# Kernel tuning notes

Measured on AMD Instinct MI355X. Metric: run time of the kernel, lower is better.

The kernel has to match this reference:

```python
import jax, jax.numpy as jnp
import numpy as np

OBJECTNESS_LIMIT = 0.7
NUM_ANCHORS = 9
DN = ('NHWC', 'HWIO', 'NHWC')


def _conv(x, w, b):
    return jax.lax.conv_general_dilated(x, w, (1, 1), 'SAME', dimension_numbers=DN) + b


def setup_inputs() -> dict:
    key = jax.random.key(0)
    ks = jax.random.split(key, 4)
    B, H, W, Cin = 4, 256, 256, 64
    x = jax.random.normal(ks[0], (B, H, W, Cin), dtype=jnp.float32)
    # base: Conv2D(512, 3x3, relu, kernel_initializer='normal')
    w_base = jax.random.normal(ks[1], (3, 3, Cin, 512), dtype=jnp.float32) * 0.02
    b_base = jnp.zeros((512,), dtype=jnp.float32)
    # classifier: Conv2D(9, 1x1, sigmoid, kernel_initializer='uniform')
    w_cls = jax.random.uniform(ks[2], (1, 1, 512, NUM_ANCHORS), dtype=jnp.float32, minval=-0.05, maxval=0.05)
    b_cls = jnp.zeros((NUM_ANCHORS,), dtype=jnp.float32)
    w_reg = jax.random.normal(ks[3], (1, 1, 512, 4 * NUM_ANCHORS), dtype=jnp.float32) * 0.02
    b_reg = jnp.zeros((4 * NUM_ANCHORS,), dtype=jnp.float32)
    return {"x": x, "w_base": w_base, "b_base": b_base,
            "w_cls": w_cls, "b_cls": b_cls, "w_reg": w_reg, "b_reg": b_reg}


def reference(x, w_base, b_base, w_cls, b_cls, w_reg, b_reg):
    # shared 3x3 conv trunk
    feat = jax.nn.relu(_conv(x, w_base, b_base))                 # [B,H,W,512]
    # per-anchor objectness
    scores = jax.nn.sigmoid(_conv(feat, w_cls, b_cls))           # [B,H,W,A]
    deltas = _conv(feat, w_reg, b_reg)                           # [B,H,W,4A]
    B, H, W, A = scores.shape
    # vectorized form of the per-anchor threshold loop: keep deltas only
    # where objectness > limit (gather/filter expressed as a mask)
    mask = (scores > OBJECTNESS_LIMIT).astype(deltas.dtype)      # [B,H,W,A]
    masked = (deltas.reshape(B, H, W, A, 4) * mask[..., None]).reshape(B, H, W, 4 * A)
    return jnp.concatenate([scores, masked], axis=-1)            # [B,H,W,5A]
```

## Files before the change

kernel.cpp:

```cpp
#include <hip/hip_runtime.h>
#include <hip/hip_bf16.h>
#include <math.h>


typedef _Float16 fp16x8 __attribute__((ext_vector_type(8)));
typedef _Float16 fp16x4 __attribute__((ext_vector_type(4)));
typedef float    f32x4  __attribute__((ext_vector_type(4)));

#define BT_ELEMS  (18 * 32 * 64 * 8)
#define BT2_ELEMS (48 * 512)
#define BS_BYTES  32768

__global__ __launch_bounds__(256) void rpn_prep(
    const float* __restrict__ wb,
    const float* __restrict__ wc,
    const float* __restrict__ wr,
    _Float16* __restrict__ btI,
    _Float16* __restrict__ bt2_hi, _Float16* __restrict__ bt2_lo)
{
    int t = blockIdx.x * 256 + threadIdx.x;
    if (t < BT_ELEMS) {
        int e    = t & 7;
        int lane = (t >> 3) & 63;
        int j    = (t >> 9) & 31;
        int s    = t >> 14;
        int wv   = j >> 3, l = j & 7;
        int lr   = lane & 15, q = lane >> 4;
        int n    = wv * 128 + l * 16 + lr;
        int k    = s * 32 + q * 8 + e;
        int tap  = k >> 6, c = k & 63;
        btI[t] = (_Float16)wb[(tap * 64 + c) * 512 + n];
    } else if (t < BT_ELEMS + BT2_ELEMS) {
        int jj = t - BT_ELEMS;
        int k = jj & 511;
        int o = jj >> 9;
        float v = 0.f;
        if (o < 9)       v = wc[k * 9 + o];
        else if (o < 45) v = wr[k * 36 + (o - 9)];
        _Float16 h = (_Float16)v;
        bt2_hi[jj] = h;
        bt2_lo[jj] = (_Float16)(v - (float)h);
    }
}

#define FB_OFF      6144
#define FB_PER_WAVE 4608
#define ARENA_BYTES 24576

#define TRUNK_STEP(S, BREG)                                                   \
    {                                                                         \
        const int tap_ = (S) >> 1;                                            \
        const int ky_  = tap_ / 3;                                            \
        const int kx_  = tap_ - ky_ * 3;                                      \
        const int c0_  = ((S) & 1) * 32 + q * 8;                              \
        fp16x8 ah[2];                                                         \
        _Pragma("unroll")                                                     \
        for (int km = 0; km < 2; ++km) {                                      \
            int rowp = km + ky_;                                              \
            int pos  = lr + kx_;                                              \
            ah[km] = *(const fp16x8*)&xs_hi[(rowp * 18 + pos) * 72 + c0_];    \
        }                                                                     \
        _Pragma("unroll")                                                     \
        for (int l = 0; l < 8; ++l) {                                         \
            acc[0][l] = __builtin_amdgcn_mfma_f32_16x16x32_f16(ah[0], BREG[l], acc[0][l], 0, 0, 0); \
            acc[1][l] = __builtin_amdgcn_mfma_f32_16x16x32_f16(ah[1], BREG[l], acc[1][l], 0, 0, 0); \
        }                                                                     \
    }

__global__ __launch_bounds__(256, 3) void rpn_main(
    const float* __restrict__ x,
    const float* __restrict__ b_base,
    const float* __restrict__ b_cls,
    const float* __restrict__ b_reg,
    const _Float16* __restrict__ btI,
    const _Float16* __restrict__ bt2_hi, const _Float16* __restrict__ bt2_lo,
    float* __restrict__ out)
{
    __shared__ char smem[ARENA_BYTES];
    _Float16* xs_hi = (_Float16*)smem;
    float*    zbuf  = (float*)smem;

    const int tid  = threadIdx.x;
    const int wave = tid >> 6;
    const int lane = tid & 63;
    const int q    = lane >> 4;
    const int lr   = lane & 15;
    const int n0   = wave * 128;

    const int wg  = blockIdx.x;
    const int b   = wg >> 11;
    const int rem = wg & 2047;
    const int h0  = (rem >> 4) * 2;
    const int w0  = (rem & 15) * 16;

    const char* gW = (const char*)btI + wave * 8192 + lane * 16;

    fp16x8 bA[8], bB[8];
    #pragma unroll
    for (int l = 0; l < 8; ++l)
        bA[l] = *(const fp16x8*)(gW + (size_t)l * 1024);

    for (int i = 0; i < 5; ++i) {
        int flat = tid + i * 256;
        if (flat < 4 * 18 * 16) {
            int cq  = flat & 15;
            int rp  = flat >> 4;
            int row = rp / 18;
            int pos = rp - row * 18;
            int hh  = h0 - 1 + row;
            int ww  = w0 - 1 + pos;
            fp16x4 h4;
            if (hh >= 0 && hh < 256 && ww >= 0 && ww < 256) {
                const float4 v = *(const float4*)&x[(((b * 256 + hh) * 256 + ww) * 64 + cq * 4)];
                h4[0] = (_Float16)v.x; h4[1] = (_Float16)v.y;
                h4[2] = (_Float16)v.z; h4[3] = (_Float16)v.w;
            } else {
                #pragma unroll
                for (int j = 0; j < 4; ++j) h4[j] = (_Float16)0.f;
            }
            *(fp16x4*)&xs_hi[(row * 18 + pos) * 72 + cq * 4] = h4;
        }
    }
    __syncthreads();

    f32x4 acc[2][8];
    #pragma unroll
    for (int km = 0; km < 2; ++km)
        #pragma unroll
        for (int l = 0; l < 8; ++l)
            acc[km][l] = (f32x4){0.f, 0.f, 0.f, 0.f};

    for (int s = 0; s < 18; s += 2) {
        {
            const char* g1 = gW + (size_t)(s + 1) * BS_BYTES;
            #pragma unroll
            for (int l = 0; l < 8; ++l)
                bB[l] = *(const fp16x8*)(g1 + (size_t)l * 1024);
        }
        TRUNK_STEP(s, bA);
        if (s + 2 < 18) {
            const char* g2 = gW + (size_t)(s + 2) * BS_BYTES;
            #pragma unroll
            for (int l = 0; l < 8; ++l)
                bA[l] = *(const fp16x8*)(g2 + (size_t)l * 1024);
        }
        TRUNK_STEP(s + 1, bB);
    }

    __syncthreads();

    _Float16* fh = (_Float16*)(smem + FB_OFF + wave * FB_PER_WAVE);
    _Float16* fl = fh + 32 * 36;

    f32x4 acc2[2][3];
    #pragma unroll
    for (int km = 0; km < 2; ++km)
        #pragma unroll
        for (int ns = 0; ns < 3; ++ns)
            acc2[km][ns] = (f32x4){0.f, 0.f, 0.f, 0.f};

    for (int sub = 0; sub < 4; ++sub) {
        #pragma unroll
        for (int lh = 0; lh < 2; ++lh) {
            int l = sub * 2 + lh;
            float bias = b_base[n0 + l * 16 + lr];
            #pragma unroll
            for (int km = 0; km < 2; ++km) {
                #pragma unroll
                for (int r = 0; r < 4; ++r) {
                    float v = acc[km][l][r] + bias;
                    v = v > 0.f ? v : 0.f;
                    _Float16 h = (_Float16)v;
                    int row = km * 16 + q * 4 + r;
                    int col = lh * 16 + lr;
                    fh[row * 36 + col] = h;
                    fl[row * 36 + col] = (_Float16)(v - (float)h);
                }
            }
        }
        asm volatile("s_waitcnt lgkmcnt(0)" ::: "memory");

        fp16x8 fah[2], fal[2];
        #pragma unroll
        for (int km = 0; km < 2; ++km) {
            int off = (km * 16 + lr) * 36 + q * 8;
            union { fp16x8 v8; fp16x4 v4[2]; } uh, ul;
            uh.v4[0] = *(const fp16x4*)&fh[off];
            uh.v4[1] = *(const fp16x4*)&fh[off + 4];
            ul.v4[0] = *(const fp16x4*)&fl[off];
            ul.v4[1] = *(const fp16x4*)&fl[off + 4];
            fah[km] = uh.v8;
            fal[km] = ul.v8;
        }

        const int kg = n0 + sub * 32 + q * 8;
        {
            int eo = (0 * 16 + lr) * 512 + kg;
            fp16x8 wh = *(const fp16x8*)&bt2_hi[eo];
            fp16x8 wl = *(const fp16x8*)&bt2_lo[eo];
            #pragma unroll
            for (int km = 0; km < 2; ++km)
                acc2[km][0] = __builtin_amdgcn_mfma_f32_16x16x32_f16(fah[km], wh, acc2[km][0], 0, 0, 0);
            #pragma unroll
            for (int km = 0; km < 2; ++km)
                acc2[km][0] = __builtin_amdgcn_mfma_f32_16x16x32_f16(fah[km], wl, acc2[km][0], 0, 0, 0);
            #pragma unroll
            for (int km = 0; km < 2; ++km)
                acc2[km][0] = __builtin_amdgcn_mfma_f32_16x16x32_f16(fal[km], wh, acc2[km][0], 0, 0, 0);
        }
        #pragma unroll
        for (int ns = 1; ns < 3; ++ns) {
            int eo = (ns * 16 + lr) * 512 + kg;
            fp16x8 wh = *(const fp16x8*)&bt2_hi[eo];
            #pragma unroll
            for (int km = 0; km < 2; ++km)
                acc2[km][ns] = __builtin_amdgcn_mfma_f32_16x16x32_f16(fah[km], wh, acc2[km][ns], 0, 0, 0);
            #pragma unroll
            for (int km = 0; km < 2; ++km)
                acc2[km][ns] = __builtin_amdgcn_mfma_f32_16x16x32_f16(fal[km], wh, acc2[km][ns], 0, 0, 0);
        }
    }

    for (int w = 0; w < 4; ++w) {
        if (wave == w) {
            #pragma unroll
            for (int km = 0; km < 2; ++km)
                #pragma unroll
                for (int ns = 0; ns < 3; ++ns)
                    #pragma unroll
                    for (int r = 0; r < 4; ++r) {
                        int row = km * 16 + q * 4 + r;
                        int col = ns * 16 + lr;
                        float v = acc2[km][ns][r];
                        if (w == 0) zbuf[row * 48 + col] = v;
                        else        zbuf[row * 48 + col] += v;
                    }
        }
        __syncthreads();
    }

    for (int i = tid; i < 32 * 45; i += 256) {
        int m = i / 45;
        int o = i - m * 45;
        float z = zbuf[m * 48 + o];
        float v;
        if (o < 9) {
            v = 1.f / (1.f + expf(-(z + b_cls[o])));
        } else {
            int d = o - 9;
            int a = d >> 2;
            float s = 1.f / (1.f + expf(-(zbuf[m * 48 + a] + b_cls[a])));
            v = (s > 0.7f) ? (z + b_reg[d]) : 0.f;
        }
        int mh = m >> 4, mw = m & 15;
        out[(((b * 256 + h0 + mh) * 256) + w0 + mw) * 45 + o] = v;
    }
}

extern "C" void kernel_launch(void* const* d_in, const int* in_sizes, int n_in,
                              void* d_out, int out_size, void* d_ws, size_t ws_size,
                              hipStream_t stream)
{
    const float* x      = (const float*)d_in[0];
    const float* w_base = (const float*)d_in[1];
    const float* b_base = (const float*)d_in[2];
    const float* w_cls  = (const float*)d_in[3];
    const float* b_cls  = (const float*)d_in[4];
    const float* w_reg  = (const float*)d_in[5];
    const float* b_reg  = (const float*)d_in[6];
    float* out = (float*)d_out;

    _Float16* btI    = (_Float16*)d_ws;
    _Float16* bt2_hi = btI + BT_ELEMS;
    _Float16* bt2_lo = bt2_hi + BT2_ELEMS;

    rpn_prep<<<(BT_ELEMS + BT2_ELEMS + 255) / 256, 256, 0, stream>>>(
        w_base, w_cls, w_reg, btI, bt2_hi, bt2_lo);
    rpn_main<<<8192, 256, 0, stream>>>(
        x, b_base, b_cls, b_reg, btI, bt2_hi, bt2_lo, out);
}
```

Before: 392.5 us.

## Pad LDS input stride, raise MFMA priority, and parallelize cross-wave reduction

Changes the LDS row stride for the staged input tile from 72 to 76 halves to reduce bank conflicts on the A-fragment reads. Wraps the MFMA loop of each trunk step in s_setprio so waves issuing matrix work get scheduling priority. Replaces the four-pass serialized cross-wave accumulation into one buffer, which took four barriers, with per-wave slices written in parallel and summed during the epilogue. The feature buffers now start at offset 0 and the arena grows slightly, which may affect occupancy at 3 blocks per CU.

```diff
diff --git a/kernel.cpp b/kernel.cpp
--- a/kernel.cpp
+++ b/kernel.cpp
@@ -43,9 +43,10 @@
     }
 }
 
-#define FB_OFF      6144
+#define XS_STRIDE   76
 #define FB_PER_WAVE 4608
-#define ARENA_BYTES 24576
+#define ZB_SLICE    1600
+#define ARENA_BYTES 25600
 
 #define TRUNK_STEP(S, BREG)                                                   \
     {                                                                         \
@@ -58,13 +59,15 @@
         for (int km = 0; km < 2; ++km) {                                      \
             int rowp = km + ky_;                                              \
             int pos  = lr + kx_;                                              \
-            ah[km] = *(const fp16x8*)&xs_hi[(rowp * 18 + pos) * 72 + c0_];    \
+            ah[km] = *(const fp16x8*)&xs_hi[(rowp * 18 + pos) * XS_STRIDE + c0_]; \
         }                                                                     \
+        __builtin_amdgcn_s_setprio(1);                                        \
         _Pragma("unroll")                                                     \
         for (int l = 0; l < 8; ++l) {                                         \
             acc[0][l] = __builtin_amdgcn_mfma_f32_16x16x32_f16(ah[0], BREG[l], acc[0][l], 0, 0, 0); \
             acc[1][l] = __builtin_amdgcn_mfma_f32_16x16x32_f16(ah[1], BREG[l], acc[1][l], 0, 0, 0); \
         }                                                                     \
+        __builtin_amdgcn_s_setprio(0);                                        \
     }
 
 __global__ __launch_bounds__(256, 3) void rpn_main(
@@ -78,7 +81,7 @@
 {
     __shared__ char smem[ARENA_BYTES];
     _Float16* xs_hi = (_Float16*)smem;
-    float*    zbuf  = (float*)smem;
+    float*    zb    = (float*)smem;
 
     const int tid  = threadIdx.x;
     const int wave = tid >> 6;
@@ -118,7 +121,7 @@
                 #pragma unroll
                 for (int j = 0; j < 4; ++j) h4[j] = (_Float16)0.f;
             }
-            *(fp16x4*)&xs_hi[(row * 18 + pos) * 72 + cq * 4] = h4;
+            *(fp16x4*)&xs_hi[(row * 18 + pos) * XS_STRIDE + cq * 4] = h4;
         }
     }
     __syncthreads();
@@ -149,7 +152,7 @@
 
     __syncthreads();
 
-    _Float16* fh = (_Float16*)(smem + FB_OFF + wave * FB_PER_WAVE);
+    _Float16* fh = (_Float16*)(smem + wave * FB_PER_WAVE);
     _Float16* fl = fh + 32 * 36;
 
     f32x4 acc2[2][3];
@@ -221,35 +224,37 @@
         }
     }
 
-    for (int w = 0; w < 4; ++w) {
-        if (wave == w) {
-            #pragma unroll
-            for (int km = 0; km < 2; ++km)
+    __syncthreads();
+
+    {
+        float* zw = zb + wave * ZB_SLICE;
+        #pragma unroll
+        for (int km = 0; km < 2; ++km)
+            #pragma unroll
+            for (int ns = 0; ns < 3; ++ns)
                 #pragma unroll
-                for (int ns = 0; ns < 3; ++ns)
-                    #pragma unroll
-                    for (int r = 0; r < 4; ++r) {
-                        int row = km * 16 + q * 4 + r;
-                        int col = ns * 16 + lr;
-                        float v = acc2[km][ns][r];
-                        if (w == 0) zbuf[row * 48 + col] = v;
-                        else        zbuf[row * 48 + col] += v;
-                    }
-        }
-        __syncthreads();
-    }
+                for (int r = 0; r < 4; ++r) {
+                    int row = km * 16 + q * 4 + r;
+                    int col = ns * 16 + lr;
+                    zw[row * 50 + col] = acc2[km][ns][r];
+                }
+    }
+    __syncthreads();
 
     for (int i = tid; i < 32 * 45; i += 256) {
         int m = i / 45;
         int o = i - m * 45;
-        float z = zbuf[m * 48 + o];
+        int e0 = m * 50 + o;
+        float z = ((zb[e0] + zb[ZB_SLICE + e0]) + zb[2 * ZB_SLICE + e0]) + zb[3 * ZB_SLICE + e0];
         float v;
         if (o < 9) {
             v = 1.f / (1.f + expf(-(z + b_cls[o])));
         } else {
             int d = o - 9;
             int a = d >> 2;
-            float s = 1.f / (1.f + expf(-(zbuf[m * 48 + a] + b_cls[a])));
+            int ea = m * 50 + a;
+            float za = ((zb[ea] + zb[ZB_SLICE + ea]) + zb[2 * ZB_SLICE + ea]) + zb[3 * ZB_SLICE + ea];
+            float s = 1.f / (1.f + expf(-(za + b_cls[a])));
             v = (s > 0.7f) ? (z + b_reg[d]) : 0.f;
         }
         int mh = m >> 4, mw = m & 15;
```

After: 360.6 us. 8.1% less time.
